# Kernel optimization log

Hardware: AMD Instinct MI355X
Metric: run time of the kernel (lower is better)

Reference implementation:

```python
import jax, jax.numpy as jnp
import numpy as np

NUM_CLASSES = 91
NUM_ANCHORS = 3234
VAR_XY, VAR_WH = 0.1, 0.2
SCORE_THRESH = 0.05
NMS_THRESH = 0.5
PRE_NMS_TOPK = 200  # original default 400; reduced to bound the [C-1,K,K] IoU buffer
MAX_DET = 100
BATCH = 64


def _xyxy_to_cxcywh(b):
    wh = b[..., 2:] - b[..., :2]
    c = b[..., :2] + 0.5 * wh
    return jnp.concatenate([c, wh], axis=-1)


def _pairwise_iou(b):
    # b: [K,4] xyxy -> [K,K] IoU
    lt = jnp.maximum(b[:, None, :2], b[None, :, :2])
    rb = jnp.minimum(b[:, None, 2:], b[None, :, 2:])
    inter = jnp.prod(jnp.clip(rb - lt, 0.0), axis=-1)
    area = jnp.prod(jnp.clip(b[:, 2:] - b[:, :2], 0.0), axis=-1)
    union = area[:, None] + area[None, :] - inter
    return inter / jnp.maximum(union, 1e-9)


def _nms_keep(boxes):
    # boxes [K,4] already sorted by descending score; greedy NMS keep mask [K]
    K = boxes.shape[0]
    iou = _pairwise_iou(jax.lax.stop_gradient(boxes))
    idx = jnp.arange(K)

    def body(i, keep):
        suppress = keep[i] & (iou[i] > NMS_THRESH) & (idx > i)
        return keep & ~suppress

    return jax.lax.fori_loop(0, K, body, jnp.ones((K,), dtype=bool))


def setup_inputs() -> dict:
    key = jax.random.key(0)
    k1, k2, k3, k4 = jax.random.split(key, 4)
    cls_logits = jax.random.normal(k1, (BATCH, NUM_ANCHORS, NUM_CLASSES), dtype=jnp.float32)
    box_reg = jax.random.normal(k2, (BATCH, NUM_ANCHORS, 4), dtype=jnp.float32)
    # valid normalized anchor boxes in xyxy
    cxy = jax.random.uniform(k3, (NUM_ANCHORS, 2), minval=0.05, maxval=0.95)
    wh = jax.random.uniform(k4, (NUM_ANCHORS, 2), minval=0.02, maxval=0.4)
    priors = jnp.concatenate([cxy - wh / 2, cxy + wh / 2], axis=-1).astype(jnp.float32)
    return {"cls_logits": cls_logits, "box_reg": box_reg, "priors": priors}


def reference(cls_logits, box_reg, priors):
    probs = jax.nn.softmax(cls_logits, axis=-1)           # [B,A,C]
    pr_c = _xyxy_to_cxcywh(priors)                        # [A,4]

    def per_image(args):
        loc, p = args                                     # [A,4], [A,C]
        # _decode with variances (0.1, 0.2)
        xy = loc[:, :2] * VAR_XY * pr_c[:, 2:] + pr_c[:, :2]
        wh = jnp.exp(loc[:, 2:] * VAR_WH) * pr_c[:, 2:]
        boxes = jnp.concatenate([xy - wh / 2, xy + wh / 2], axis=-1)  # [A,4]

        scores_c = p[:, 1:].T                             # [C-1, A], skip background
        vals, idx = jax.lax.top_k(scores_c, PRE_NMS_TOPK)  # [C-1,K] sorted desc
        boxes_c = boxes[idx]                              # [C-1,K,4]
        keep = jax.vmap(_nms_keep)(boxes_c)               # [C-1,K]
        valid = vals > SCORE_THRESH
        fscores = jnp.where(keep & valid, vals, 0.0)      # masked-out dets scored 0
        labels = jnp.broadcast_to(
            jnp.arange(1, NUM_CLASSES, dtype=jnp.float32)[:, None], fscores.shape)

        flat_s = fscores.reshape(-1)
        flat_b = boxes_c.reshape(-1, 4)
        flat_l = labels.reshape(-1)
        top_s, top_i = jax.lax.top_k(flat_s, MAX_DET)     # global top-100 by score
        preds = jnp.concatenate(
            [flat_b[top_i], top_s[:, None], flat_l[top_i, None]], axis=-1)  # [100,6]
        return jnp.where(top_s[:, None] > 0, preds, 0.0)  # zero padding rows

    return jax.lax.map(per_image, (box_reg, probs))        # [B,100,6]
```

## Files before the change

kernel.cpp:

```cpp
#include <hip/hip_runtime.h>
#include <cstdint>

#define NCLS 91
#define NA   3234
#define NB   64
#define KTOP 200
#define CAP  192
#define MAXDET 100
#define NCM1 90
#define CAPI 8192
#define LCAP 768
#define NBIN 1024
#define BOFF 0x3D4C
#define FBUF 1024

typedef unsigned long long u64;
typedef unsigned int u32;


__device__ __forceinline__ u64 u64max(u64 a, u64 b) { return a > b ? a : b; }
__device__ __forceinline__ u64 u64min(u64 a, u64 b) { return a < b ? a : b; }

__device__ __forceinline__ u64 shfl_xor_u64(u64 v, int m) {
  int lo = __shfl_xor((int)(u32)v, m, 64);
  int hi = __shfl_xor((int)(u32)(v >> 32), m, 64);
  return ((u64)(u32)hi << 32) | (u32)lo;
}

template <int SLOTS>
__device__ __forceinline__ void bitonic_desc(u64* key, int t) {
  const int N = SLOTS * 64;
  for (int k = 2; k <= N; k <<= 1) {
    for (int j = k >> 1; j > 0; j >>= 1) {
      if (j >= 64) {
        int sj = j >> 6;
        #pragma unroll
        for (int s = 0; s < SLOTS; ++s) {
          int sp = s ^ sj;
          if (sp > s) {
            int e = s * 64 + t;
            bool up = ((e & k) == 0);
            u64 a = key[s], b = key[sp];
            u64 mx = u64max(a, b), mn = u64min(a, b);
            key[s]  = up ? mx : mn;
            key[sp] = up ? mn : mx;
          }
        }
      } else {
        #pragma unroll
        for (int s = 0; s < SLOTS; ++s) {
          int e = s * 64 + t;
          u64 p = shfl_xor_u64(key[s], j);
          bool up = ((e & k) == 0);
          bool lower = ((t & j) == 0);
          key[s] = (up == lower) ? u64max(key[s], p) : u64min(key[s], p);
        }
      }
    }
  }
}

__global__ __launch_bounds__(256, 2) void prep_kernel(
    const float* __restrict__ logits, const float* __restrict__ box_reg,
    const float* __restrict__ priors, float* __restrict__ boxes,
    u64* __restrict__ cand, int* __restrict__ cnt) {
  __shared__ u64 lkey[LCAP];
  __shared__ unsigned short lbc[LCAP];
  __shared__ int lcnt;
  int t = threadIdx.x;
  if (t == 0) lcnt = 0;
  __syncthreads();

  int i = blockIdx.x * 256 + t;
  bool act = (i < NB * NA);
  int b = 0, a = 0;
  float ssum = 1.f, thr = 1e30f;
  float h1e = 0.f, h2e = 0.f;
  float4 r[22];
  float q0e = 0.f, q1e = 0.f, q2e = 0.f;
  int al = t & 3, nt = 3 - al;

  if (act) {
    b = i / NA; a = i - b * NA;

    float4 pr = ((const float4*)priors)[a];
    float pw = pr.z - pr.x, ph = pr.w - pr.y;
    float cx = pr.x + 0.5f * pw, cy = pr.y + 0.5f * ph;
    float4 lc = ((const float4*)box_reg)[i];
    float x = lc.x * 0.1f * pw + cx;
    float y = lc.y * 0.1f * ph + cy;
    float bw = expf(lc.z * 0.2f) * pw;
    float bh = expf(lc.w * 0.2f) * ph;
    float4 bxo;
    bxo.x = x - bw * 0.5f; bxo.y = y - bh * 0.5f;
    bxo.z = x + bw * 0.5f; bxo.w = y + bh * 0.5f;
    ((float4*)boxes)[i] = bxo;

    const float* lp = logits + (size_t)i * NCLS;
    const float4* cv = (const float4*)(lp + al);
    float h0 = 0.f, h1 = 0.f, h2 = 0.f;
    if (al > 0) h0 = lp[0];
    if (al > 1) h1 = lp[1];
    if (al > 2) h2 = lp[2];
    #pragma unroll
    for (int v = 0; v < 22; ++v) r[v] = cv[v];
    float q0 = 0.f, q1 = 0.f, q2 = 0.f;
    if (nt > 0) q0 = lp[al + 88];
    if (nt > 1) q1 = lp[al + 89];
    if (nt > 2) q2 = lp[al + 90];

    float m = -3.402823466e38f;
    if (al > 0) m = fmaxf(m, h0);
    if (al > 1) m = fmaxf(m, h1);
    if (al > 2) m = fmaxf(m, h2);
    #pragma unroll
    for (int v = 0; v < 22; ++v) {
      float4 q = r[v];
      m = fmaxf(m, fmaxf(fmaxf(q.x, q.y), fmaxf(q.z, q.w)));
    }
    if (nt > 0) m = fmaxf(m, q0);
    if (nt > 1) m = fmaxf(m, q1);
    if (nt > 2) m = fmaxf(m, q2);

    ssum = 0.f;
    if (al > 0) ssum += expf(h0 - m);
    if (al > 1) { h1e = expf(h1 - m); ssum += h1e; }
    if (al > 2) { h2e = expf(h2 - m); ssum += h2e; }
    #pragma unroll
    for (int v = 0; v < 22; ++v) {
      float4 q = r[v];
      float e0 = expf(q.x - m), e1 = expf(q.y - m);
      float e2 = expf(q.z - m), e3 = expf(q.w - m);
      ssum += e0; ssum += e1; ssum += e2; ssum += e3;
      r[v] = make_float4(e0, e1, e2, e3);
    }
    if (nt > 0) { q0e = expf(q0 - m); ssum += q0e; }
    if (nt > 1) { q1e = expf(q1 - m); ssum += q1e; }
    if (nt > 2) { q2e = expf(q2 - m); ssum += q2e; }
    thr = 0.05f * ssum;
  }

  u64 abits = (u64)(u32)(~a);
  int bb90 = b * NCM1;
  #define PUSH(E, CC) do { \
    float _e = (E); \
    if (_e > thr) { \
      int _lp = atomicAdd(&lcnt, 1); \
      if (_lp < LCAP) { \
        lkey[_lp] = ((u64)__float_as_uint(_e / ssum) << 32) | abits; \
        lbc[_lp] = (unsigned short)(bb90 + (CC) - 1); \
      } \
    } \
  } while (0)

  if (act) {
    if (al > 1) PUSH(h1e, 1);
    if (al > 2) PUSH(h2e, 2);
    #pragma unroll
    for (int v = 0; v < 22; ++v) {
      float4 q = r[v];
      int cb = al + 4 * v;
      if (v != 0 || al != 0) PUSH(q.x, cb);
      PUSH(q.y, cb + 1);
      PUSH(q.z, cb + 2);
      PUSH(q.w, cb + 3);
    }
    if (nt > 0) PUSH(q0e, al + 88);
    if (nt > 1) PUSH(q1e, al + 89);
    if (nt > 2) PUSH(q2e, al + 90);
  }
  #undef PUSH
  __syncthreads();

  int nL = lcnt; if (nL > LCAP) nL = LCAP;
  for (int j = t; j < nL; j += 256) {
    int bcv = lbc[j];
    int pos = atomicAdd(&cnt[bcv], 1);
    if (pos < CAP) cand[(size_t)bcv * CAP + pos] = lkey[j];
  }
}

__global__ __launch_bounds__(256) void sort_nms_kernel(
    const u64* __restrict__ cand, const int* __restrict__ cnt,
    const float* __restrict__ boxes,
    u64* __restrict__ img_keys, int* __restrict__ img_cnt) {
  __shared__ float4 sbx[4][CAP];
  int w = threadIdx.x >> 6;
  int t = threadIdx.x & 63;
  int bc = blockIdx.x * 4 + w;
  int b = bc / NCM1;
  int cm1 = bc - b * NCM1;

  int n = cnt[bc]; if (n > CAP) n = CAP;

  u64 key[4];
  #pragma unroll
  for (int s = 0; s < 4; ++s) {
    int e = s * 64 + t;
    key[s] = (e < n) ? cand[(size_t)bc * CAP + e] : 0ULL;
  }
  if (n <= 64)       bitonic_desc<1>(key, t);
  else if (n <= 128) bitonic_desc<2>(key, t);
  else               bitonic_desc<4>(key, t);

  float4 bx[3];
  #pragma unroll
  for (int s = 0; s < 3; ++s) {
    int rr = s * 64 + t;
    if (rr < n) {
      int a = (int)(~(u32)key[s]);
      float4 bbx = ((const float4*)boxes)[b * NA + a];
      bx[s] = bbx;
      sbx[w][rr] = bbx;
    }
  }
  __syncthreads();

  u64 m00 = 0, m10 = 0, m11 = 0, m20 = 0, m21 = 0, m22 = 0;
  #pragma unroll
  for (int T = 0; T < 3; ++T) {
    int rr = T * 64 + t;
    if (rr < n) {
      float4 bi = bx[T];
      float ai = fmaxf(bi.z - bi.x, 0.f) * fmaxf(bi.w - bi.y, 0.f);
      for (int s = 0; s < rr; ++s) {
        float4 bj = sbx[w][s];
        float xx1 = fmaxf(bi.x, bj.x), yy1 = fmaxf(bi.y, bj.y);
        float xx2 = fminf(bi.z, bj.z), yy2 = fminf(bi.w, bj.w);
        float inter = fmaxf(xx2 - xx1, 0.f) * fmaxf(yy2 - yy1, 0.f);
        float aj = fmaxf(bj.z - bj.x, 0.f) * fmaxf(bj.w - bj.y, 0.f);
        float iou = inter / fmaxf(ai + aj - inter, 1e-9f);
        if (iou > 0.5f) {
          u64 bit = 1ull << (s & 63);
          int wd = s >> 6;
          if (T == 0)      { m00 |= bit; }
          else if (T == 1) { if (wd == 0) m10 |= bit; else m11 |= bit; }
          else             { if (wd == 0) m20 |= bit; else if (wd == 1) m21 |= bit; else m22 |= bit; }
        }
      }
    }
  }

  int a0 = 1, a1 = 1, a2 = 1;
  int lim = n < 64 ? n : 64;
  for (int i = 0; i < lim; ++i) {
    if (__shfl(a0, i, 64)) {
      a0 &= ~(int)((m00 >> i) & 1ull);
      a1 &= ~(int)((m10 >> i) & 1ull);
      a2 &= ~(int)((m20 >> i) & 1ull);
    }
  }
  lim = n - 64; if (lim > 64) lim = 64;
  for (int i = 0; i < lim; ++i) {
    if (__shfl(a1, i, 64)) {
      a1 &= ~(int)((m11 >> i) & 1ull);
      a2 &= ~(int)((m21 >> i) & 1ull);
    }
  }
  lim = n - 128; if (lim > 64) lim = 64;
  for (int i = 0; i < lim; ++i) {
    if (__shfl(a2, i, 64)) a2 &= ~(int)((m22 >> i) & 1ull);
  }

  u64 av0 = __ballot(a0 && (t < n));
  u64 av1 = __ballot(a1 && (64 + t < n));
  u64 av2 = __ballot(a2 && (128 + t < n));
  int c0 = __popcll(av0), c1 = __popcll(av1), c2 = __popcll(av2);
  int tot = c0 + c1 + c2;
  int base = 0;
  if (t == 0 && tot) base = atomicAdd(&img_cnt[b], tot);
  base = __shfl(base, 0, 64);
  u64 lmlt = (1ull << t) - 1ull;
  int alv[3] = {a0, a1, a2};
  u64 avs[3] = {av0, av1, av2};
  int pres[3] = {0, c0, c0 + c1};
  #pragma unroll
  for (int s = 0; s < 3; ++s) {
    int rr = s * 64 + t;
    if (alv[s] && rr < n) {
      int pos = base + pres[s] + __popcll(avs[s] & lmlt);
      if (pos < CAPI) {
        u32 sbits = (u32)(key[s] >> 32);
        int fidx = cm1 * KTOP + rr;
        int anch = (int)(~(u32)key[s]);
        img_keys[(size_t)b * CAPI + pos] =
            ((u64)sbits << 27) | ((u64)(u32)(0x7FFF - fidx) << 12) | (u64)(u32)anch;
      }
    }
  }
}

__global__ __launch_bounds__(1024) void topdet_kernel(
    const u64* __restrict__ img_keys, const int* __restrict__ img_cnt,
    const float* __restrict__ boxes, float* __restrict__ out) {
  __shared__ int hist[NBIN];
  __shared__ u64 buf[FBUF];
  __shared__ int part[256];
  __shared__ int sh_nsel, sh_T;
  int b = blockIdx.x, t = threadIdx.x;
  int n = img_cnt[b]; if (n > CAPI) n = CAPI;

  for (int i = t; i < NBIN; i += 1024) hist[i] = 0;
  if (t == 0) { sh_nsel = 0; sh_T = 0; }
  __syncthreads();

  for (int i = t; i < n; i += 1024) {
    int bin = (int)(img_keys[(size_t)b * CAPI + i] >> 43) - BOFF;
    bin = bin < 0 ? 0 : (bin > NBIN - 1 ? NBIN - 1 : bin);
    atomicAdd(&hist[bin], 1);
  }
  __syncthreads();

  int b0 = 0, psum = 0, v = 0;
  if (t < 256) {
    b0 = NBIN - 1 - 4 * t;
    psum = hist[b0] + hist[b0 - 1] + hist[b0 - 2] + hist[b0 - 3];
    v = psum;
    part[t] = v;
  }
  __syncthreads();
  for (int d = 1; d < 256; d <<= 1) {
    int add = (t < 256 && t >= d) ? part[t - d] : 0;
    __syncthreads();
    if (t < 256) { v += add; part[t] = v; }
    __syncthreads();
  }
  if (t < 256) {
    int above = v - psum;
    if (above < MAXDET && v >= MAXDET) {
      int acc = above;
      for (int k = 0; k < 4; ++k) {
        acc += hist[b0 - k];
        if (acc >= MAXDET) { sh_T = b0 - k; break; }
      }
    }
  }
  __syncthreads();

  int T = sh_T;
  for (int i = t; i < n; i += 1024) {
    u64 key = img_keys[(size_t)b * CAPI + i];
    int bin = (int)(key >> 43) - BOFF;
    bin = bin < 0 ? 0 : (bin > NBIN - 1 ? NBIN - 1 : bin);
    if (bin >= T) {
      int pos = atomicAdd(&sh_nsel, 1);
      if (pos < FBUF) buf[pos] = key;
    }
  }
  __syncthreads();

  int ns = sh_nsel; if (ns > FBUF) ns = FBUF;

  if (ns <= 256) {
    if (t < 64) {
      u64 key[4];
      #pragma unroll
      for (int s = 0; s < 4; ++s) {
        int e = s * 64 + t;
        key[s] = (e < ns) ? buf[e] : 0ULL;
      }
      if (ns <= 128) bitonic_desc<2>(key, t);
      else           bitonic_desc<4>(key, t);
      buf[t] = key[0];
      if (t < 36) buf[64 + t] = key[1];
    }
    __syncthreads();
  } else {
    int npow = 1; while (npow < ns) npow <<= 1;
    for (int i = t; i < npow; i += 1024) if (i >= ns) buf[i] = 0ULL;
    __syncthreads();
    for (int k = 2; k <= npow; k <<= 1) {
      for (int j = k >> 1; j > 0; j >>= 1) {
        for (int i = t; i < npow; i += 1024) {
          int l = i ^ j;
          if (l > i) {
            u64 x0 = buf[i], x1 = buf[l];
            bool up = ((i & k) == 0);
            if (up ? (x0 < x1) : (x0 > x1)) { buf[i] = x1; buf[l] = x0; }
          }
        }
        __syncthreads();
      }
    }
  }

  if (t < MAXDET) {
    float* row = out + ((size_t)b * MAXDET + t) * 6;
    if (t < ns) {
      u64 key = buf[t];
      float vsc = __uint_as_float((u32)(key >> 27));
      int fidx = 0x7FFF - (int)((key >> 12) & 0x7FFF);
      int a = (int)(key & 0xFFF);
      float4 bb = ((const float4*)boxes)[b * NA + a];
      row[0] = bb.x; row[1] = bb.y; row[2] = bb.z; row[3] = bb.w;
      row[4] = vsc;
      row[5] = (float)(fidx / KTOP + 1);
    } else {
      row[0] = 0.f; row[1] = 0.f; row[2] = 0.f;
      row[3] = 0.f; row[4] = 0.f; row[5] = 0.f;
    }
  }
}

extern "C" void kernel_launch(void* const* d_in, const int* in_sizes, int n_in,
                              void* d_out, int out_size, void* d_ws, size_t ws_size,
                              hipStream_t stream) {
  const float* logits  = (const float*)d_in[0];
  const float* box_reg = (const float*)d_in[1];
  const float* priors  = (const float*)d_in[2];
  float* out = (float*)d_out;

  char* ws = (char*)d_ws;
  size_t off = 0;
  float* boxes = (float*)(ws + off);               off += (size_t)NB * NA * 4 * sizeof(float);
  u64* cand = (u64*)(ws + off);                    off += (size_t)NB * NCM1 * CAP * sizeof(u64);
  u64* img_keys = (u64*)(ws + off);                off += (size_t)NB * CAPI * sizeof(u64);
  int* cnt = (int*)(ws + off);                     off += (size_t)NB * NCM1 * sizeof(int);
  int* img_cnt = (int*)(ws + off);                 off += (size_t)NB * sizeof(int);
  (void)ws_size; (void)in_sizes; (void)n_in; (void)out_size;

  hipMemsetAsync(cnt, 0, (size_t)(NB * NCM1 + NB) * sizeof(int), stream);
  prep_kernel<<<(NB * NA + 255) / 256, 256, 0, stream>>>(
      logits, box_reg, priors, boxes, cand, cnt);
  sort_nms_kernel<<<NB * NCM1 / 4, 256, 0, stream>>>(
      cand, cnt, boxes, img_keys, img_cnt);
  topdet_kernel<<<NB, 1024, 0, stream>>>(img_keys, img_cnt, boxes, out);
}
```

Before: 242.2 us.

## Shrink prep blocks, log-domain threshold, rank-sort and forward-mask NMS in shared memory

The prep kernel now runs 64-thread blocks with a smaller local buffer. It drops the stored exponentials and instead compares each logit minus the max against log(0.05*sum), recomputing exp only for candidates that pass. The sort+NMS kernel replaces the bitonic sort with an O(n^2) shuffle rank count and scatters the sorted keys and boxes into shared memory. It then builds forward suppression masks in shared memory and resolves them with a serial per-row loop instead of shuffles. The aim is to cut register pressure and sort cost, at the price of recomputed exps, quadratic ranking, and larger shared-memory use.

```diff
diff --git a/kernel.cpp b/kernel.cpp
--- a/kernel.cpp
+++ b/kernel.cpp
@@ -9,7 +9,7 @@
 #define MAXDET 100
 #define NCM1 90
 #define CAPI 8192
-#define LCAP 768
+#define LCAP 256
 #define NBIN 1024
 #define BOFF 0x3D4C
 #define FBUF 1024
@@ -24,6 +24,11 @@
 __device__ __forceinline__ u64 shfl_xor_u64(u64 v, int m) {
   int lo = __shfl_xor((int)(u32)v, m, 64);
   int hi = __shfl_xor((int)(u32)(v >> 32), m, 64);
+  return ((u64)(u32)hi << 32) | (u32)lo;
+}
+__device__ __forceinline__ u64 shfl_u64(u64 v, int src) {
+  int lo = __shfl((int)(u32)v, src, 64);
+  int hi = __shfl((int)(u32)(v >> 32), src, 64);
   return ((u64)(u32)hi << 32) | (u32)lo;
 }
 
@@ -60,7 +65,7 @@
   }
 }
 
-__global__ __launch_bounds__(256, 2) void prep_kernel(
+__global__ __launch_bounds__(64) void prep_kernel(
     const float* __restrict__ logits, const float* __restrict__ box_reg,
     const float* __restrict__ priors, float* __restrict__ boxes,
     u64* __restrict__ cand, int* __restrict__ cnt) {
@@ -71,80 +76,72 @@
   if (t == 0) lcnt = 0;
   __syncthreads();
 
-  int i = blockIdx.x * 256 + t;
-  bool act = (i < NB * NA);
-  int b = 0, a = 0;
-  float ssum = 1.f, thr = 1e30f;
-  float h1e = 0.f, h2e = 0.f;
+  int i = blockIdx.x * 64 + t;
+  int b = i / NA, a = i - b * NA;
+
+  float4 pr = ((const float4*)priors)[a];
+  float pw = pr.z - pr.x, ph = pr.w - pr.y;
+  float cx = pr.x + 0.5f * pw, cy = pr.y + 0.5f * ph;
+  float4 lc = ((const float4*)box_reg)[i];
+  float x = lc.x * 0.1f * pw + cx;
+  float y = lc.y * 0.1f * ph + cy;
+  float bw = expf(lc.z * 0.2f) * pw;
+  float bh = expf(lc.w * 0.2f) * ph;
+  float4 bxo;
+  bxo.x = x - bw * 0.5f; bxo.y = y - bh * 0.5f;
+  bxo.z = x + bw * 0.5f; bxo.w = y + bh * 0.5f;
+  ((float4*)boxes)[i] = bxo;
+
+  const float* lp = logits + (size_t)i * NCLS;
+  int al = t & 3, nt = 3 - al;
+  const float4* cv = (const float4*)(lp + al);
+
+  float h0 = 0.f, h1 = 0.f, h2 = 0.f;
+  if (al > 0) h0 = lp[0];
+  if (al > 1) h1 = lp[1];
+  if (al > 2) h2 = lp[2];
   float4 r[22];
-  float q0e = 0.f, q1e = 0.f, q2e = 0.f;
-  int al = t & 3, nt = 3 - al;
-
-  if (act) {
-    b = i / NA; a = i - b * NA;
-
-    float4 pr = ((const float4*)priors)[a];
-    float pw = pr.z - pr.x, ph = pr.w - pr.y;
-    float cx = pr.x + 0.5f * pw, cy = pr.y + 0.5f * ph;
-    float4 lc = ((const float4*)box_reg)[i];
-    float x = lc.x * 0.1f * pw + cx;
-    float y = lc.y * 0.1f * ph + cy;
-    float bw = expf(lc.z * 0.2f) * pw;
-    float bh = expf(lc.w * 0.2f) * ph;
-    float4 bxo;
-    bxo.x = x - bw * 0.5f; bxo.y = y - bh * 0.5f;
-    bxo.z = x + bw * 0.5f; bxo.w = y + bh * 0.5f;
-    ((float4*)boxes)[i] = bxo;
-
-    const float* lp = logits + (size_t)i * NCLS;
-    const float4* cv = (const float4*)(lp + al);
-    float h0 = 0.f, h1 = 0.f, h2 = 0.f;
-    if (al > 0) h0 = lp[0];
-    if (al > 1) h1 = lp[1];
-    if (al > 2) h2 = lp[2];
-    #pragma unroll
-    for (int v = 0; v < 22; ++v) r[v] = cv[v];
-    float q0 = 0.f, q1 = 0.f, q2 = 0.f;
-    if (nt > 0) q0 = lp[al + 88];
-    if (nt > 1) q1 = lp[al + 89];
-    if (nt > 2) q2 = lp[al + 90];
-
-    float m = -3.402823466e38f;
-    if (al > 0) m = fmaxf(m, h0);
-    if (al > 1) m = fmaxf(m, h1);
-    if (al > 2) m = fmaxf(m, h2);
-    #pragma unroll
-    for (int v = 0; v < 22; ++v) {
-      float4 q = r[v];
-      m = fmaxf(m, fmaxf(fmaxf(q.x, q.y), fmaxf(q.z, q.w)));
-    }
-    if (nt > 0) m = fmaxf(m, q0);
-    if (nt > 1) m = fmaxf(m, q1);
-    if (nt > 2) m = fmaxf(m, q2);
-
-    ssum = 0.f;
-    if (al > 0) ssum += expf(h0 - m);
-    if (al > 1) { h1e = expf(h1 - m); ssum += h1e; }
-    if (al > 2) { h2e = expf(h2 - m); ssum += h2e; }
-    #pragma unroll
-    for (int v = 0; v < 22; ++v) {
-      float4 q = r[v];
-      float e0 = expf(q.x - m), e1 = expf(q.y - m);
-      float e2 = expf(q.z - m), e3 = expf(q.w - m);
-      ssum += e0; ssum += e1; ssum += e2; ssum += e3;
-      r[v] = make_float4(e0, e1, e2, e3);
-    }
-    if (nt > 0) { q0e = expf(q0 - m); ssum += q0e; }
-    if (nt > 1) { q1e = expf(q1 - m); ssum += q1e; }
-    if (nt > 2) { q2e = expf(q2 - m); ssum += q2e; }
-    thr = 0.05f * ssum;
-  }
-
+  #pragma unroll
+  for (int v = 0; v < 22; ++v) r[v] = cv[v];
+  float q0 = 0.f, q1 = 0.f, q2 = 0.f;
+  if (nt > 0) q0 = lp[al + 88];
+  if (nt > 1) q1 = lp[al + 89];
+  if (nt > 2) q2 = lp[al + 90];
+
+  float m = -3.402823466e38f;
+  if (al > 0) m = fmaxf(m, h0);
+  if (al > 1) m = fmaxf(m, h1);
+  if (al > 2) m = fmaxf(m, h2);
+  #pragma unroll
+  for (int v = 0; v < 22; ++v) {
+    float4 q = r[v];
+    m = fmaxf(m, fmaxf(fmaxf(q.x, q.y), fmaxf(q.z, q.w)));
+  }
+  if (nt > 0) m = fmaxf(m, q0);
+  if (nt > 1) m = fmaxf(m, q1);
+  if (nt > 2) m = fmaxf(m, q2);
+
+  float ssum = 0.f;
+  if (al > 0) ssum += expf(h0 - m);
+  if (al > 1) ssum += expf(h1 - m);
+  if (al > 2) ssum += expf(h2 - m);
+  #pragma unroll
+  for (int v = 0; v < 22; ++v) {
+    float4 q = r[v];
+    ssum += expf(q.x - m); ssum += expf(q.y - m);
+    ssum += expf(q.z - m); ssum += expf(q.w - m);
+  }
+  if (nt > 0) ssum += expf(q0 - m);
+  if (nt > 1) ssum += expf(q1 - m);
+  if (nt > 2) ssum += expf(q2 - m);
+
+  float lthr = logf(0.05f * ssum);
   u64 abits = (u64)(u32)(~a);
   int bb90 = b * NCM1;
-  #define PUSH(E, CC) do { \
-    float _e = (E); \
-    if (_e > thr) { \
+  #define PUSH(L, CC) do { \
+    float _d = (L) - m; \
+    if (_d > lthr) { \
+      float _e = expf(_d); \
       int _lp = atomicAdd(&lcnt, 1); \
       if (_lp < LCAP) { \
         lkey[_lp] = ((u64)__float_as_uint(_e / ssum) << 32) | abits; \
@@ -153,27 +150,25 @@
     } \
   } while (0)
 
-  if (act) {
-    if (al > 1) PUSH(h1e, 1);
-    if (al > 2) PUSH(h2e, 2);
-    #pragma unroll
-    for (int v = 0; v < 22; ++v) {
-      float4 q = r[v];
-      int cb = al + 4 * v;
-      if (v != 0 || al != 0) PUSH(q.x, cb);
-      PUSH(q.y, cb + 1);
-      PUSH(q.z, cb + 2);
-      PUSH(q.w, cb + 3);
-    }
-    if (nt > 0) PUSH(q0e, al + 88);
-    if (nt > 1) PUSH(q1e, al + 89);
-    if (nt > 2) PUSH(q2e, al + 90);
-  }
+  if (al > 1) PUSH(h1, 1);
+  if (al > 2) PUSH(h2, 2);
+  #pragma unroll
+  for (int v = 0; v < 22; ++v) {
+    float4 q = r[v];
+    int cb = al + 4 * v;
+    if (v != 0 || al != 0) PUSH(q.x, cb);
+    PUSH(q.y, cb + 1);
+    PUSH(q.z, cb + 2);
+    PUSH(q.w, cb + 3);
+  }
+  if (nt > 0) PUSH(q0, al + 88);
+  if (nt > 1) PUSH(q1, al + 89);
+  if (nt > 2) PUSH(q2, al + 90);
   #undef PUSH
   __syncthreads();
 
   int nL = lcnt; if (nL > LCAP) nL = LCAP;
-  for (int j = t; j < nL; j += 256) {
+  for (int j = t; j < nL; j += 64) {
     int bcv = lbc[j];
     int pos = atomicAdd(&cnt[bcv], 1);
     if (pos < CAP) cand[(size_t)bcv * CAP + pos] = lkey[j];
@@ -184,7 +179,9 @@
     const u64* __restrict__ cand, const int* __restrict__ cnt,
     const float* __restrict__ boxes,
     u64* __restrict__ img_keys, int* __restrict__ img_cnt) {
+  __shared__ u64 sk[4][CAP];
   __shared__ float4 sbx[4][CAP];
+  __shared__ u64 sm[4][CAP][3];
   int w = threadIdx.x >> 6;
   int t = threadIdx.x & 63;
   int bc = blockIdx.x * 4 + w;
@@ -193,98 +190,96 @@
 
   int n = cnt[bc]; if (n > CAP) n = CAP;
 
-  u64 key[4];
-  #pragma unroll
-  for (int s = 0; s < 4; ++s) {
+  u64 key[3];
+  #pragma unroll
+  for (int s = 0; s < 3; ++s) {
     int e = s * 64 + t;
     key[s] = (e < n) ? cand[(size_t)bc * CAP + e] : 0ULL;
   }
-  if (n <= 64)       bitonic_desc<1>(key, t);
-  else if (n <= 128) bitonic_desc<2>(key, t);
-  else               bitonic_desc<4>(key, t);
-
-  float4 bx[3];
+
+  int rk0 = 0, rk1 = 0, rk2 = 0;
+  for (int s = 0; s < n; ++s) {
+    u64 ks = shfl_u64(key[s >> 6], s & 63);
+    rk0 += (ks > key[0]);
+    rk1 += (ks > key[1]);
+    rk2 += (ks > key[2]);
+  }
+  int rks[3] = {rk0, rk1, rk2};
+
   #pragma unroll
   for (int s = 0; s < 3; ++s) {
-    int rr = s * 64 + t;
-    if (rr < n) {
+    int e = s * 64 + t;
+    if (e < n) {
+      int rr = rks[s];
+      sk[w][rr] = key[s];
       int a = (int)(~(u32)key[s]);
-      float4 bbx = ((const float4*)boxes)[b * NA + a];
-      bx[s] = bbx;
-      sbx[w][rr] = bbx;
-    }
-  }
-  __syncthreads();
-
-  u64 m00 = 0, m10 = 0, m11 = 0, m20 = 0, m21 = 0, m22 = 0;
+      sbx[w][rr] = ((const float4*)boxes)[b * NA + a];
+    }
+  }
+  __syncthreads();
+
   #pragma unroll
   for (int T = 0; T < 3; ++T) {
     int rr = T * 64 + t;
     if (rr < n) {
-      float4 bi = bx[T];
+      float4 bi = sbx[w][rr];
       float ai = fmaxf(bi.z - bi.x, 0.f) * fmaxf(bi.w - bi.y, 0.f);
-      for (int s = 0; s < rr; ++s) {
-        float4 bj = sbx[w][s];
+      u64 m0 = 0, m1 = 0, m2 = 0;
+      for (int j = rr + 1; j < n; ++j) {
+        float4 bj = sbx[w][j];
         float xx1 = fmaxf(bi.x, bj.x), yy1 = fmaxf(bi.y, bj.y);
         float xx2 = fminf(bi.z, bj.z), yy2 = fminf(bi.w, bj.w);
         float inter = fmaxf(xx2 - xx1, 0.f) * fmaxf(yy2 - yy1, 0.f);
         float aj = fmaxf(bj.z - bj.x, 0.f) * fmaxf(bj.w - bj.y, 0.f);
         float iou = inter / fmaxf(ai + aj - inter, 1e-9f);
         if (iou > 0.5f) {
-          u64 bit = 1ull << (s & 63);
-          int wd = s >> 6;
-          if (T == 0)      { m00 |= bit; }
-          else if (T == 1) { if (wd == 0) m10 |= bit; else m11 |= bit; }
-          else             { if (wd == 0) m20 |= bit; else if (wd == 1) m21 |= bit; else m22 |= bit; }
+          u64 bit = 1ull << (j & 63);
+          int wd = j >> 6;
+          if (wd == 0) m0 |= bit; else if (wd == 1) m1 |= bit; else m2 |= bit;
         }
       }
-    }
-  }
-
-  int a0 = 1, a1 = 1, a2 = 1;
-  int lim = n < 64 ? n : 64;
-  for (int i = 0; i < lim; ++i) {
-    if (__shfl(a0, i, 64)) {
-      a0 &= ~(int)((m00 >> i) & 1ull);
-      a1 &= ~(int)((m10 >> i) & 1ull);
-      a2 &= ~(int)((m20 >> i) & 1ull);
-    }
-  }
-  lim = n - 64; if (lim > 64) lim = 64;
-  for (int i = 0; i < lim; ++i) {
-    if (__shfl(a1, i, 64)) {
-      a1 &= ~(int)((m11 >> i) & 1ull);
-      a2 &= ~(int)((m21 >> i) & 1ull);
-    }
-  }
-  lim = n - 128; if (lim > 64) lim = 64;
-  for (int i = 0; i < lim; ++i) {
-    if (__shfl(a2, i, 64)) a2 &= ~(int)((m22 >> i) & 1ull);
-  }
-
-  u64 av0 = __ballot(a0 && (t < n));
-  u64 av1 = __ballot(a1 && (64 + t < n));
-  u64 av2 = __ballot(a2 && (128 + t < n));
-  int c0 = __popcll(av0), c1 = __popcll(av1), c2 = __popcll(av2);
+      sm[w][rr][0] = m0; sm[w][rr][1] = m1; sm[w][rr][2] = m2;
+    }
+  }
+  __syncthreads();
+
+  u64 kp0 = ~0ull, kp1 = ~0ull, kp2 = ~0ull;
+  for (int iidx = 0; iidx < n; ++iidx) {
+    u64 s0 = sm[w][iidx][0], s1 = sm[w][iidx][1], s2 = sm[w][iidx][2];
+    u64 kw = (iidx < 64) ? kp0 : (iidx < 128) ? kp1 : kp2;
+    u64 live = 0ull - ((kw >> (iidx & 63)) & 1ull);
+    kp0 &= ~(s0 & live); kp1 &= ~(s1 & live); kp2 &= ~(s2 & live);
+  }
+
+  auto rng = [](int mm, int wd) -> u64 {
+    int c = mm - wd * 64;
+    if (c <= 0) return 0ull;
+    if (c >= 64) return ~0ull;
+    return (1ull << c) - 1ull;
+  };
+  u64 k0 = kp0 & rng(n, 0), k1 = kp1 & rng(n, 1), k2 = kp2 & rng(n, 2);
+  int c0 = __popcll(k0), c1 = __popcll(k1), c2 = __popcll(k2);
   int tot = c0 + c1 + c2;
   int base = 0;
   if (t == 0 && tot) base = atomicAdd(&img_cnt[b], tot);
   base = __shfl(base, 0, 64);
-  u64 lmlt = (1ull << t) - 1ull;
-  int alv[3] = {a0, a1, a2};
-  u64 avs[3] = {av0, av1, av2};
-  int pres[3] = {0, c0, c0 + c1};
-  #pragma unroll
-  for (int s = 0; s < 3; ++s) {
-    int rr = s * 64 + t;
-    if (alv[s] && rr < n) {
-      int pos = base + pres[s] + __popcll(avs[s] & lmlt);
-      if (pos < CAPI) {
-        u32 sbits = (u32)(key[s] >> 32);
-        int fidx = cm1 * KTOP + rr;
-        int anch = (int)(~(u32)key[s]);
-        img_keys[(size_t)b * CAPI + pos] =
-            ((u64)sbits << 27) | ((u64)(u32)(0x7FFF - fidx) << 12) | (u64)(u32)anch;
+  if (tot) {
+    u64 lmlt = (1ull << t) - 1ull;
+    u64 kws[3] = {k0, k1, k2};
+    int pres[3] = {0, c0, c0 + c1};
+    #pragma unroll
+    for (int s = 0; s < 3; ++s) {
+      int rr = s * 64 + t;
+      if (rr < n && ((kws[s] >> t) & 1ull)) {
+        int pos = base + pres[s] + __popcll(kws[s] & lmlt);
+        if (pos < CAPI) {
+          u64 kk = sk[w][rr];
+          u32 sbits = (u32)(kk >> 32);
+          int fidx = cm1 * KTOP + rr;
+          int anch = (int)(~(u32)kk);
+          img_keys[(size_t)b * CAPI + pos] =
+              ((u64)sbits << 27) | ((u64)(u32)(0x7FFF - fidx) << 12) | (u64)(u32)anch;
+        }
       }
     }
   }
@@ -420,7 +415,7 @@
   (void)ws_size; (void)in_sizes; (void)n_in; (void)out_size;
 
   hipMemsetAsync(cnt, 0, (size_t)(NB * NCM1 + NB) * sizeof(int), stream);
-  prep_kernel<<<(NB * NA + 255) / 256, 256, 0, stream>>>(
+  prep_kernel<<<NB * NA / 64, 64, 0, stream>>>(
       logits, box_reg, priors, boxes, cand, cnt);
   sort_nms_kernel<<<NB * NCM1 / 4, 256, 0, stream>>>(
       cand, cnt, boxes, img_keys, img_cnt);
```

New measurement: 254.7 us. 1.05x slower.
